# Performance work log

Hardware: AMD Instinct MI355X
Metric: run time of the kernel (lower is better)

## Reference

```python
import jax, jax.numpy as jnp
import numpy as np

N_NODES = 100000
EPS = 1e-6
NEG_SLOPE = 0.2


def setup_inputs() -> dict:
    key = jax.random.key(0)
    ks = jax.random.split(key, 7)
    N, E, IN, H, F = N_NODES, 1600000, 128, 4, 32
    feat = jax.random.normal(ks[0], (N, IN), dtype=jnp.float32)
    src = jax.random.randint(ks[1], (E,), 0, N, dtype=jnp.int32)
    dst = jax.random.randint(ks[2], (E,), 0, N, dtype=jnp.int32)
    # xavier-normal-ish scales (gain for relu = sqrt(2))
    W = jax.random.normal(ks[3], (IN, H * F), dtype=jnp.float32) * np.sqrt(2.0 * 2.0 / (IN + H * F)).astype(np.float32)
    attn_l = jax.random.normal(ks[4], (1, H, F), dtype=jnp.float32) * np.float32(np.sqrt(2.0 * 2.0 / (1 + F)))
    attn_r = jax.random.normal(ks[5], (1, H, F), dtype=jnp.float32) * np.float32(np.sqrt(2.0 * 2.0 / (1 + F)))
    bias = jnp.zeros((H * F,), dtype=jnp.float32)
    p = jax.random.normal(ks[6], (1,), dtype=jnp.float32)
    s_f = jnp.ones((1,), dtype=jnp.float32)
    return {"feat": feat, "src": src, "dst": dst, "W": W, "attn_l": attn_l,
            "attn_r": attn_r, "bias": bias, "p": p, "s_f": s_f}


def _leaky_relu(x, slope):
    return jnp.where(x >= 0, x, slope * x)


def reference(feat, src, dst, W, attn_l, attn_r, bias, p, s_f):
    N, H, F = feat.shape[0], attn_l.shape[1], attn_l.shape[2]
    # linear projection: [N, H, F]
    feat_proj = (feat @ W).reshape(N, H, F)
    # per-node attention logits: [N, H]
    el = jnp.sum(feat_proj * attn_l, axis=-1)
    er = jnp.sum(feat_proj * attn_r, axis=-1)
    # edge logits e = leaky_relu(el[src] + er[dst]) : [E, H]
    e = _leaky_relu(el[src] + er[dst], NEG_SLOPE)
    # edge softmax over incoming edges of each destination node
    emax = jax.ops.segment_max(e, dst, num_segments=N)        # [N, H]
    emax = jnp.where(jnp.isfinite(emax), emax, 0.0)
    e_exp = jnp.exp(e - emax[dst])                            # [E, H]
    denom = jax.ops.segment_sum(e_exp, dst, num_segments=N)   # [N, H]
    a = e_exp / (denom[dst] + 0.0)                            # [E, H]
    # power-mean aggregation
    p_eff = jax.nn.sigmoid(p[0]) + s_f[0]
    mu = feat_proj.min()
    pre_f = jnp.power(feat_proj - mu + EPS, p_eff)            # [N, H, F]
    msg = pre_f[src] * a[:, :, None]                          # [E, H, F]
    pre_rst = jax.ops.segment_sum(msg, dst, num_segments=N)   # [N, H, F]
    rst = jnp.power(pre_rst + EPS, 1.0 / p_eff) + mu
    rst = rst + bias.reshape(1, H, F)
    return rst.reshape(N, H * F)
```

## Files before the change

kernel.cpp:

```cpp
#include <hip/hip_runtime.h>
#include <hip/hip_fp16.h>
#include <math.h>

#define EPS 1e-6f
#define SLOPE 0.2f
#define NPART 8
#define BK 64

typedef __attribute__((ext_vector_type(8))) _Float16 f16x8;
typedef __attribute__((ext_vector_type(4))) float f32x4;

__device__ __forceinline__ unsigned fmap(float f) {
    unsigned b = __float_as_uint(f);
    return (b & 0x80000000u) ? ~b : (b | 0x80000000u);
}
__device__ __forceinline__ float funmap(unsigned m) {
    unsigned b = (m & 0x80000000u) ? (m ^ 0x80000000u) : ~m;
    return __uint_as_float(b);
}

__global__ __launch_bounds__(256) void gemm_mfma_kernel(
    const float* __restrict__ feat, const float* __restrict__ W,
    const float* __restrict__ attn_l, const float* __restrict__ attn_r,
    __half* __restrict__ fph, float* __restrict__ el, float* __restrict__ er,
    unsigned* __restrict__ mu_m, int N)
{
    __shared__ ushort Ald[128][136];
    __shared__ ushort Wld[128][136];
    __shared__ float red[256];

    int tid = threadIdx.x;
    int n0 = blockIdx.x * 128;

#pragma unroll
    for (int rep = 0; rep < 8; ++rep) {
        int slot = tid + rep * 256;
        int row = slot >> 4;
        int k8 = (slot & 15) << 3;
        int gr = n0 + row;
        uint4 u = make_uint4(0u, 0u, 0u, 0u);
        if (gr < N) {
            const float4* f4 = (const float4*)(feat + (size_t)gr * 128 + k8);
            float4 va = f4[0], vb = f4[1];
            __half2 p0 = __floats2half2_rn(va.x, va.y);
            __half2 p1 = __floats2half2_rn(va.z, va.w);
            __half2 p2 = __floats2half2_rn(vb.x, vb.y);
            __half2 p3 = __floats2half2_rn(vb.z, vb.w);
            u.x = *reinterpret_cast<unsigned*>(&p0);
            u.y = *reinterpret_cast<unsigned*>(&p1);
            u.z = *reinterpret_cast<unsigned*>(&p2);
            u.w = *reinterpret_cast<unsigned*>(&p3);
        }
        *(uint4*)&Ald[row][k8] = u;
    }
#pragma unroll
    for (int rep = 0; rep < 8; ++rep) {
        int slot = tid + rep * 256;
        int col = slot & 127;
        int k0 = (slot >> 7) << 3;
        ushort h[8];
#pragma unroll
        for (int j = 0; j < 8; ++j)
            h[j] = __half_as_ushort(__float2half_rn(W[(size_t)(k0 + j) * 128 + col]));
        *(uint4*)&Wld[col][k0] = *(uint4*)h;
    }
    __syncthreads();

    int lane = tid & 63;
    int wid = tid >> 6;
    int wr = wid >> 1, wc = wid & 1;
    int cl = lane & 15, g = lane >> 4;

    f32x4 acc[4][4];
#pragma unroll
    for (int i = 0; i < 4; i++)
#pragma unroll
        for (int j = 0; j < 4; j++) acc[i][j] = (f32x4){0.f, 0.f, 0.f, 0.f};

#pragma unroll
    for (int ks = 0; ks < 4; ++ks) {
        int kk = ks * 32 + g * 8;
        f16x8 aF[4], bF[4];
#pragma unroll
        for (int rt = 0; rt < 4; ++rt)
            aF[rt] = *(const f16x8*)&Ald[wr * 64 + rt * 16 + cl][kk];
#pragma unroll
        for (int ct = 0; ct < 4; ++ct)
            bF[ct] = *(const f16x8*)&Wld[wc * 64 + ct * 16 + cl][kk];
#pragma unroll
        for (int rt = 0; rt < 4; ++rt)
#pragma unroll
            for (int ct = 0; ct < 4; ++ct)
                acc[rt][ct] = __builtin_amdgcn_mfma_f32_16x16x32_f16(
                    aF[rt], bF[ct], acc[rt][ct], 0, 0, 0);
    }

    float alv[4], arv[4];
#pragma unroll
    for (int ct = 0; ct < 4; ++ct) {
        int h = (4 * wc + ct) >> 1;
        int f = ((ct & 1) << 4) + cl;
        alv[ct] = attn_l[h * 32 + f];
        arv[ct] = attn_r[h * 32 + f];
    }
#pragma unroll
    for (int rt = 0; rt < 4; ++rt) {
#pragma unroll
        for (int reg = 0; reg < 4; ++reg) {
            float e0 = acc[rt][0][reg] * alv[0] + acc[rt][1][reg] * alv[1];
            float e1 = acc[rt][2][reg] * alv[2] + acc[rt][3][reg] * alv[3];
            float r0 = acc[rt][0][reg] * arv[0] + acc[rt][1][reg] * arv[1];
            float r1 = acc[rt][2][reg] * arv[2] + acc[rt][3][reg] * arv[3];
#pragma unroll
            for (int m = 1; m < 16; m <<= 1) {
                e0 += __shfl_xor(e0, m);
                e1 += __shfl_xor(e1, m);
                r0 += __shfl_xor(r0, m);
                r1 += __shfl_xor(r1, m);
            }
            int R = n0 + wr * 64 + rt * 16 + g * 4 + reg;
            if (cl == 0 && R < N) {
                *(float2*)(el + (size_t)R * 4 + 2 * wc) = make_float2(e0, e1);
                *(float2*)(er + (size_t)R * 4 + 2 * wc) = make_float2(r0, r1);
            }
        }
    }

    float lmin = INFINITY;
#pragma unroll
    for (int rt = 0; rt < 4; ++rt)
#pragma unroll
        for (int reg = 0; reg < 4; ++reg) {
            int R = n0 + wr * 64 + rt * 16 + g * 4 + reg;
            if (R < N) {
#pragma unroll
                for (int ct = 0; ct < 4; ++ct) lmin = fminf(lmin, acc[rt][ct][reg]);
            }
        }
    red[tid] = lmin;
    __syncthreads();
    for (int s2 = 128; s2 > 0; s2 >>= 1) {
        if (tid < s2) red[tid] = fminf(red[tid], red[tid + s2]);
        __syncthreads();
    }
    if (tid == 0) atomicMin(mu_m, fmap(red[0]));

    __syncthreads();
    __half* hbuf = (__half*)&Ald[0][0];
#pragma unroll
    for (int rt = 0; rt < 4; ++rt)
#pragma unroll
        for (int ct = 0; ct < 4; ++ct)
#pragma unroll
            for (int reg = 0; reg < 4; ++reg) {
                int row = wr * 64 + rt * 16 + g * 4 + reg;
                int col = wc * 64 + ct * 16 + cl;
                hbuf[row * 136 + col] = __float2half_rn(acc[rt][ct][reg]);
            }
    __syncthreads();
    {
        int row = tid >> 1, seg = tid & 1;
        int gr = n0 + row;
        if (gr < N) {
            const uint4* s4 = (const uint4*)&Ald[row][seg * 64];
            uint4* d4 = (uint4*)(fph + (size_t)gr * 128 + seg * 64);
#pragma unroll
            for (int q = 0; q < 8; ++q) d4[q] = s4[q];
        }
    }
}

__global__ __launch_bounds__(256) void scatter_powp_kernel(
    const int* __restrict__ src, const int* __restrict__ dst,
    int* __restrict__ cnt, int* __restrict__ sorted_src,
    __half* __restrict__ fph, const unsigned* __restrict__ mu_m,
    const float* __restrict__ p, const float* __restrict__ s_f,
    int total8, int E, int N)
{
    {
        float mu = funmap(*mu_m);
        float pe = 1.f / (1.f + __expf(-p[0])) + s_f[0];
        int stride = gridDim.x * 256;
        for (int i = blockIdx.x * 256 + threadIdx.x; i < total8; i += stride) {
            uint4 u = *reinterpret_cast<uint4*>(fph + (size_t)i * 8);
            float2 f0 = __half22float2(*reinterpret_cast<__half2*>(&u.x));
            float2 f1 = __half22float2(*reinterpret_cast<__half2*>(&u.y));
            float2 f2 = __half22float2(*reinterpret_cast<__half2*>(&u.z));
            float2 f3 = __half22float2(*reinterpret_cast<__half2*>(&u.w));
            f0.x = __expf(pe * __logf(fmaxf(f0.x - mu, 0.f) + EPS));
            f0.y = __expf(pe * __logf(fmaxf(f0.y - mu, 0.f) + EPS));
            f1.x = __expf(pe * __logf(fmaxf(f1.x - mu, 0.f) + EPS));
            f1.y = __expf(pe * __logf(fmaxf(f1.y - mu, 0.f) + EPS));
            f2.x = __expf(pe * __logf(fmaxf(f2.x - mu, 0.f) + EPS));
            f2.y = __expf(pe * __logf(fmaxf(f2.y - mu, 0.f) + EPS));
            f3.x = __expf(pe * __logf(fmaxf(f3.x - mu, 0.f) + EPS));
            f3.y = __expf(pe * __logf(fmaxf(f3.y - mu, 0.f) + EPS));
            __half2 q0 = __floats2half2_rn(f0.x, f0.y);
            __half2 q1 = __floats2half2_rn(f1.x, f1.y);
            __half2 q2 = __floats2half2_rn(f2.x, f2.y);
            __half2 q3 = __floats2half2_rn(f3.x, f3.y);
            u.x = *reinterpret_cast<unsigned*>(&q0);
            u.y = *reinterpret_cast<unsigned*>(&q1);
            u.z = *reinterpret_cast<unsigned*>(&q2);
            u.w = *reinterpret_cast<unsigned*>(&q3);
            *reinterpret_cast<uint4*>(fph + (size_t)i * 8) = u;
        }
    }

    int grp = blockIdx.x & (NPART - 1);
    int R = (N + NPART - 1) / NPART;
    int lo = grp * R;
    int hi = min(N, lo + R);
    int E4 = E >> 2;
    int stride4 = (gridDim.x >> 3) * 256;
    const int4* dst4 = (const int4*)dst;
    const int4* src4 = (const int4*)src;
    for (int e4 = (blockIdx.x >> 3) * 256 + threadIdx.x; e4 < E4; e4 += stride4) {
        int4 d4 = dst4[e4];
        bool m0 = (d4.x >= lo) & (d4.x < hi);
        bool m1 = (d4.y >= lo) & (d4.y < hi);
        bool m2 = (d4.z >= lo) & (d4.z < hi);
        bool m3 = (d4.w >= lo) & (d4.w < hi);
        if (m0 | m1 | m2 | m3) {
            int4 s4 = src4[e4];
            if (m0) { int pos = atomicAdd(&cnt[d4.x], 1); if (pos < BK) sorted_src[(size_t)d4.x * BK + pos] = s4.x; }
            if (m1) { int pos = atomicAdd(&cnt[d4.y], 1); if (pos < BK) sorted_src[(size_t)d4.y * BK + pos] = s4.y; }
            if (m2) { int pos = atomicAdd(&cnt[d4.z], 1); if (pos < BK) sorted_src[(size_t)d4.z * BK + pos] = s4.z; }
            if (m3) { int pos = atomicAdd(&cnt[d4.w], 1); if (pos < BK) sorted_src[(size_t)d4.w * BK + pos] = s4.w; }
        }
    }
    if (blockIdx.x < NPART) {
        for (int e = E4 * 4 + threadIdx.x; e < E; e += 256) {
            int d = dst[e];
            if (d >= lo && d < hi) {
                int pos = atomicAdd(&cnt[d], 1);
                if (pos < BK) sorted_src[(size_t)d * BK + pos] = src[e];
            }
        }
    }
}

__global__ __launch_bounds__(256) void agg_kernel(
    const int* __restrict__ sorted_src, const int* __restrict__ cnt,
    const float* __restrict__ el, const float* __restrict__ er,
    const __half* __restrict__ fph, const float* __restrict__ bias,
    const unsigned* __restrict__ mu_m, const float* __restrict__ p,
    const float* __restrict__ s_f, float* __restrict__ out, int N)
{
    int node = blockIdx.x * 4 + (threadIdx.x >> 6);
    int lane = threadIdx.x & 63;
    if (node >= N) return;
    int esel = lane >> 3;
    int fb = lane & 7;
    int h = fb >> 1;
    float er_h = er[(size_t)node * 4 + h];

    int len = min(cnt[node], BK);
    int base = node * BK;

    float a[16];
#pragma unroll
    for (int q = 0; q < 16; q++) a[q] = 0.f;
    float dn = 0.f;

    for (int i = 0; i < len; i += 8) {
        int j = i + esel;
        bool valid = (j < len);
        int s = sorted_src[base + (valid ? j : i)];

        float x = el[(size_t)s * 4 + h] + er_h;
        x = x >= 0.f ? x : SLOPE * x;
        float w = valid ? __expf(x) : 0.f;
        uint4 u0 = *(const uint4*)(fph + (size_t)s * 128 + fb * 16);
        uint4 u1 = *(const uint4*)(fph + (size_t)s * 128 + fb * 16 + 8);
        dn += w;
        float2 gg;
        gg = __half22float2(*reinterpret_cast<__half2*>(&u0.x)); a[0]  = fmaf(w, gg.x, a[0]);  a[1]  = fmaf(w, gg.y, a[1]);
        gg = __half22float2(*reinterpret_cast<__half2*>(&u0.y)); a[2]  = fmaf(w, gg.x, a[2]);  a[3]  = fmaf(w, gg.y, a[3]);
        gg = __half22float2(*reinterpret_cast<__half2*>(&u0.z)); a[4]  = fmaf(w, gg.x, a[4]);  a[5]  = fmaf(w, gg.y, a[5]);
        gg = __half22float2(*reinterpret_cast<__half2*>(&u0.w)); a[6]  = fmaf(w, gg.x, a[6]);  a[7]  = fmaf(w, gg.y, a[7]);
        gg = __half22float2(*reinterpret_cast<__half2*>(&u1.x)); a[8]  = fmaf(w, gg.x, a[8]);  a[9]  = fmaf(w, gg.y, a[9]);
        gg = __half22float2(*reinterpret_cast<__half2*>(&u1.y)); a[10] = fmaf(w, gg.x, a[10]); a[11] = fmaf(w, gg.y, a[11]);
        gg = __half22float2(*reinterpret_cast<__half2*>(&u1.z)); a[12] = fmaf(w, gg.x, a[12]); a[13] = fmaf(w, gg.y, a[13]);
        gg = __half22float2(*reinterpret_cast<__half2*>(&u1.w)); a[14] = fmaf(w, gg.x, a[14]); a[15] = fmaf(w, gg.y, a[15]);
    }

#pragma unroll
    for (int q = 0; q < 16; q++) {
        a[q] += __shfl_xor(a[q], 8);
        a[q] += __shfl_xor(a[q], 16);
        a[q] += __shfl_xor(a[q], 32);
    }
    dn += __shfl_xor(dn, 8);
    dn += __shfl_xor(dn, 16);
    dn += __shfl_xor(dn, 32);

    if (esel == 0) {
        float mu = funmap(*mu_m);
        float pe = 1.f / (1.f + __expf(-p[0])) + s_f[0];
        float ip = 1.f / pe;
        float inv_dn = (len > 0) ? (1.f / dn) : 0.f;
        float o[16];
#pragma unroll
        for (int q = 0; q < 16; q++) {
            float b = bias[fb * 16 + q];
            o[q] = __expf(ip * __logf(fmaf(a[q], inv_dn, EPS))) + mu + b;
        }
        *(float4*)(out + (size_t)node * 128 + fb * 16)      = *(float4*)(&o[0]);
        *(float4*)(out + (size_t)node * 128 + fb * 16 + 4)  = *(float4*)(&o[4]);
        *(float4*)(out + (size_t)node * 128 + fb * 16 + 8)  = *(float4*)(&o[8]);
        *(float4*)(out + (size_t)node * 128 + fb * 16 + 12) = *(float4*)(&o[12]);
    }
}

extern "C" void kernel_launch(void* const* d_in, const int* in_sizes, int n_in,
                              void* d_out, int out_size, void* d_ws, size_t ws_size,
                              hipStream_t stream)
{
    const float* feat   = (const float*)d_in[0];
    const int*   src    = (const int*)d_in[1];
    const int*   dst    = (const int*)d_in[2];
    const float* W      = (const float*)d_in[3];
    const float* attn_l = (const float*)d_in[4];
    const float* attn_r = (const float*)d_in[5];
    const float* bias   = (const float*)d_in[6];
    const float* p      = (const float*)d_in[7];
    const float* s_f    = (const float*)d_in[8];
    float* out = (float*)d_out;

    const int N = in_sizes[0] / 128;
    const int E = in_sizes[1];

    char* ws = (char*)d_ws;
    size_t off = 0;
    auto alloc = [&](size_t bytes) -> char* {
        char* ptr = ws + off;
        off = (off + bytes + 255) & ~(size_t)255;
        return ptr;
    };
    __half*   fph        = (__half*)alloc((size_t)N * 128 * 2);
    float*    el         = (float*)alloc((size_t)N * 4 * 4);
    float*    er         = (float*)alloc((size_t)N * 4 * 4);
    int*      cnt        = (int*)alloc((size_t)N * 4);
    int*      sorted_src = (int*)alloc((size_t)N * BK * 4);
    unsigned* mu_m       = (unsigned*)alloc(256);

    hipMemsetAsync(cnt,  0,    (size_t)N * 4, stream);
    hipMemsetAsync(mu_m, 0xFF, 4,             stream);

    int total8 = N * 128 / 8;

    gemm_mfma_kernel<<<(N + 127) / 128, 256, 0, stream>>>(
        feat, W, attn_l, attn_r, fph, el, er, mu_m, N);
    scatter_powp_kernel<<<2048, 256, 0, stream>>>(src, dst, cnt, sorted_src,
                                                  fph, mu_m, p, s_f, total8, E, N);
    agg_kernel<<<(N + 3) / 4, 256, 0, stream>>>(sorted_src, cnt, el, er, fph,
                                                bias, mu_m, p, s_f, out, N);
}
```

Before: 219.6 us.

## Move edge bucketing into GEMM kernel and spread agg epilogue across all lanes

The dst-bucketed edge scatter moves out of the power kernel and into the tail of the GEMM kernel. It is independent of the projection, so it can overlap with the GEMM's compute-bound work, and the power kernel becomes a pure elementwise pass. In the aggregation kernel, the reduced accumulators go through shared memory so all 64 lanes, not just 8, each finish two output columns with log/exp and write coalesced float2 stores. Risks: the GEMM kernel's register and LDS pressure goes up, and it now runs ~782 blocks instead of 2048 for the scatter. Also, the shared fin buffer is read without a __syncthreads, relying on wave-level ordering within one wavefront.

```diff
diff --git a/kernel.cpp b/kernel.cpp
--- a/kernel.cpp
+++ b/kernel.cpp
@@ -19,11 +19,13 @@
     return __uint_as_float(b);
 }
 
-__global__ __launch_bounds__(256) void gemm_mfma_kernel(
+__global__ __launch_bounds__(256) void gemm_mfma_scatter_kernel(
     const float* __restrict__ feat, const float* __restrict__ W,
     const float* __restrict__ attn_l, const float* __restrict__ attn_r,
+    const int* __restrict__ src, const int* __restrict__ dst,
+    int* __restrict__ cnt, int* __restrict__ sorted_src,
     __half* __restrict__ fph, float* __restrict__ el, float* __restrict__ er,
-    unsigned* __restrict__ mu_m, int N)
+    unsigned* __restrict__ mu_m, int N, int E)
 {
     __shared__ ushort Ald[128][136];
     __shared__ ushort Wld[128][136];
@@ -168,75 +170,74 @@
             for (int q = 0; q < 8; ++q) d4[q] = s4[q];
         }
     }
-}
-
-__global__ __launch_bounds__(256) void scatter_powp_kernel(
-    const int* __restrict__ src, const int* __restrict__ dst,
-    int* __restrict__ cnt, int* __restrict__ sorted_src,
+
+    {
+        int grp = blockIdx.x & (NPART - 1);
+        int bg = blockIdx.x >> 3;
+        int count_g = (gridDim.x + 7 - grp) >> 3;
+        int R = (N + NPART - 1) / NPART;
+        int lo = grp * R;
+        int hi = min(N, lo + R);
+        int E4 = E >> 2;
+        int stride4 = count_g * 256;
+        const int4* dst4 = (const int4*)dst;
+        const int4* src4 = (const int4*)src;
+        for (int e4 = bg * 256 + tid; e4 < E4; e4 += stride4) {
+            int4 d4 = dst4[e4];
+            bool m0 = (d4.x >= lo) & (d4.x < hi);
+            bool m1 = (d4.y >= lo) & (d4.y < hi);
+            bool m2 = (d4.z >= lo) & (d4.z < hi);
+            bool m3 = (d4.w >= lo) & (d4.w < hi);
+            if (m0 | m1 | m2 | m3) {
+                int4 s4 = src4[e4];
+                if (m0) { int pos = atomicAdd(&cnt[d4.x], 1); if (pos < BK) sorted_src[(size_t)d4.x * BK + pos] = s4.x; }
+                if (m1) { int pos = atomicAdd(&cnt[d4.y], 1); if (pos < BK) sorted_src[(size_t)d4.y * BK + pos] = s4.y; }
+                if (m2) { int pos = atomicAdd(&cnt[d4.z], 1); if (pos < BK) sorted_src[(size_t)d4.z * BK + pos] = s4.z; }
+                if (m3) { int pos = atomicAdd(&cnt[d4.w], 1); if (pos < BK) sorted_src[(size_t)d4.w * BK + pos] = s4.w; }
+            }
+        }
+        if (bg == 0) {
+            for (int e = E4 * 4 + tid; e < E; e += 256) {
+                int d = dst[e];
+                if (d >= lo && d < hi) {
+                    int pos = atomicAdd(&cnt[d], 1);
+                    if (pos < BK) sorted_src[(size_t)d * BK + pos] = src[e];
+                }
+            }
+        }
+    }
+}
+
+__global__ __launch_bounds__(256) void powp_kernel(
     __half* __restrict__ fph, const unsigned* __restrict__ mu_m,
-    const float* __restrict__ p, const float* __restrict__ s_f,
-    int total8, int E, int N)
+    const float* __restrict__ p, const float* __restrict__ s_f, int total8)
 {
-    {
-        float mu = funmap(*mu_m);
-        float pe = 1.f / (1.f + __expf(-p[0])) + s_f[0];
-        int stride = gridDim.x * 256;
-        for (int i = blockIdx.x * 256 + threadIdx.x; i < total8; i += stride) {
-            uint4 u = *reinterpret_cast<uint4*>(fph + (size_t)i * 8);
-            float2 f0 = __half22float2(*reinterpret_cast<__half2*>(&u.x));
-            float2 f1 = __half22float2(*reinterpret_cast<__half2*>(&u.y));
-            float2 f2 = __half22float2(*reinterpret_cast<__half2*>(&u.z));
-            float2 f3 = __half22float2(*reinterpret_cast<__half2*>(&u.w));
-            f0.x = __expf(pe * __logf(fmaxf(f0.x - mu, 0.f) + EPS));
-            f0.y = __expf(pe * __logf(fmaxf(f0.y - mu, 0.f) + EPS));
-            f1.x = __expf(pe * __logf(fmaxf(f1.x - mu, 0.f) + EPS));
-            f1.y = __expf(pe * __logf(fmaxf(f1.y - mu, 0.f) + EPS));
-            f2.x = __expf(pe * __logf(fmaxf(f2.x - mu, 0.f) + EPS));
-            f2.y = __expf(pe * __logf(fmaxf(f2.y - mu, 0.f) + EPS));
-            f3.x = __expf(pe * __logf(fmaxf(f3.x - mu, 0.f) + EPS));
-            f3.y = __expf(pe * __logf(fmaxf(f3.y - mu, 0.f) + EPS));
-            __half2 q0 = __floats2half2_rn(f0.x, f0.y);
-            __half2 q1 = __floats2half2_rn(f1.x, f1.y);
-            __half2 q2 = __floats2half2_rn(f2.x, f2.y);
-            __half2 q3 = __floats2half2_rn(f3.x, f3.y);
-            u.x = *reinterpret_cast<unsigned*>(&q0);
-            u.y = *reinterpret_cast<unsigned*>(&q1);
-            u.z = *reinterpret_cast<unsigned*>(&q2);
-            u.w = *reinterpret_cast<unsigned*>(&q3);
-            *reinterpret_cast<uint4*>(fph + (size_t)i * 8) = u;
-        }
-    }
-
-    int grp = blockIdx.x & (NPART - 1);
-    int R = (N + NPART - 1) / NPART;
-    int lo = grp * R;
-    int hi = min(N, lo + R);
-    int E4 = E >> 2;
-    int stride4 = (gridDim.x >> 3) * 256;
-    const int4* dst4 = (const int4*)dst;
-    const int4* src4 = (const int4*)src;
-    for (int e4 = (blockIdx.x >> 3) * 256 + threadIdx.x; e4 < E4; e4 += stride4) {
-        int4 d4 = dst4[e4];
-        bool m0 = (d4.x >= lo) & (d4.x < hi);
-        bool m1 = (d4.y >= lo) & (d4.y < hi);
-        bool m2 = (d4.z >= lo) & (d4.z < hi);
-        bool m3 = (d4.w >= lo) & (d4.w < hi);
-        if (m0 | m1 | m2 | m3) {
-            int4 s4 = src4[e4];
-            if (m0) { int pos = atomicAdd(&cnt[d4.x], 1); if (pos < BK) sorted_src[(size_t)d4.x * BK + pos] = s4.x; }
-            if (m1) { int pos = atomicAdd(&cnt[d4.y], 1); if (pos < BK) sorted_src[(size_t)d4.y * BK + pos] = s4.y; }
-            if (m2) { int pos = atomicAdd(&cnt[d4.z], 1); if (pos < BK) sorted_src[(size_t)d4.z * BK + pos] = s4.z; }
-            if (m3) { int pos = atomicAdd(&cnt[d4.w], 1); if (pos < BK) sorted_src[(size_t)d4.w * BK + pos] = s4.w; }
-        }
-    }
-    if (blockIdx.x < NPART) {
-        for (int e = E4 * 4 + threadIdx.x; e < E; e += 256) {
-            int d = dst[e];
-            if (d >= lo && d < hi) {
-                int pos = atomicAdd(&cnt[d], 1);
-                if (pos < BK) sorted_src[(size_t)d * BK + pos] = src[e];
-            }
-        }
+    float mu = funmap(*mu_m);
+    float pe = 1.f / (1.f + __expf(-p[0])) + s_f[0];
+    int stride = gridDim.x * 256;
+    for (int i = blockIdx.x * 256 + threadIdx.x; i < total8; i += stride) {
+        uint4 u = *reinterpret_cast<uint4*>(fph + (size_t)i * 8);
+        float2 f0 = __half22float2(*reinterpret_cast<__half2*>(&u.x));
+        float2 f1 = __half22float2(*reinterpret_cast<__half2*>(&u.y));
+        float2 f2 = __half22float2(*reinterpret_cast<__half2*>(&u.z));
+        float2 f3 = __half22float2(*reinterpret_cast<__half2*>(&u.w));
+        f0.x = __expf(pe * __logf(fmaxf(f0.x - mu, 0.f) + EPS));
+        f0.y = __expf(pe * __logf(fmaxf(f0.y - mu, 0.f) + EPS));
+        f1.x = __expf(pe * __logf(fmaxf(f1.x - mu, 0.f) + EPS));
+        f1.y = __expf(pe * __logf(fmaxf(f1.y - mu, 0.f) + EPS));
+        f2.x = __expf(pe * __logf(fmaxf(f2.x - mu, 0.f) + EPS));
+        f2.y = __expf(pe * __logf(fmaxf(f2.y - mu, 0.f) + EPS));
+        f3.x = __expf(pe * __logf(fmaxf(f3.x - mu, 0.f) + EPS));
+        f3.y = __expf(pe * __logf(fmaxf(f3.y - mu, 0.f) + EPS));
+        __half2 q0 = __floats2half2_rn(f0.x, f0.y);
+        __half2 q1 = __floats2half2_rn(f1.x, f1.y);
+        __half2 q2 = __floats2half2_rn(f2.x, f2.y);
+        __half2 q3 = __floats2half2_rn(f3.x, f3.y);
+        u.x = *reinterpret_cast<unsigned*>(&q0);
+        u.y = *reinterpret_cast<unsigned*>(&q1);
+        u.z = *reinterpret_cast<unsigned*>(&q2);
+        u.w = *reinterpret_cast<unsigned*>(&q3);
+        *reinterpret_cast<uint4*>(fph + (size_t)i * 8) = u;
     }
 }
 
@@ -247,9 +248,11 @@
     const unsigned* __restrict__ mu_m, const float* __restrict__ p,
     const float* __restrict__ s_f, float* __restrict__ out, int N)
 {
+    __shared__ float fin[4][8][20];
     int node = blockIdx.x * 4 + (threadIdx.x >> 6);
     int lane = threadIdx.x & 63;
     if (node >= N) return;
+    int w = threadIdx.x >> 6;
     int esel = lane >> 3;
     int fb = lane & 7;
     int h = fb >> 1;
@@ -270,19 +273,19 @@
 
         float x = el[(size_t)s * 4 + h] + er_h;
         x = x >= 0.f ? x : SLOPE * x;
-        float w = valid ? __expf(x) : 0.f;
+        float wgt = valid ? __expf(x) : 0.f;
         uint4 u0 = *(const uint4*)(fph + (size_t)s * 128 + fb * 16);
         uint4 u1 = *(const uint4*)(fph + (size_t)s * 128 + fb * 16 + 8);
-        dn += w;
+        dn += wgt;
         float2 gg;
-        gg = __half22float2(*reinterpret_cast<__half2*>(&u0.x)); a[0]  = fmaf(w, gg.x, a[0]);  a[1]  = fmaf(w, gg.y, a[1]);
-        gg = __half22float2(*reinterpret_cast<__half2*>(&u0.y)); a[2]  = fmaf(w, gg.x, a[2]);  a[3]  = fmaf(w, gg.y, a[3]);
-        gg = __half22float2(*reinterpret_cast<__half2*>(&u0.z)); a[4]  = fmaf(w, gg.x, a[4]);  a[5]  = fmaf(w, gg.y, a[5]);
-        gg = __half22float2(*reinterpret_cast<__half2*>(&u0.w)); a[6]  = fmaf(w, gg.x, a[6]);  a[7]  = fmaf(w, gg.y, a[7]);
-        gg = __half22float2(*reinterpret_cast<__half2*>(&u1.x)); a[8]  = fmaf(w, gg.x, a[8]);  a[9]  = fmaf(w, gg.y, a[9]);
-        gg = __half22float2(*reinterpret_cast<__half2*>(&u1.y)); a[10] = fmaf(w, gg.x, a[10]); a[11] = fmaf(w, gg.y, a[11]);
-        gg = __half22float2(*reinterpret_cast<__half2*>(&u1.z)); a[12] = fmaf(w, gg.x, a[12]); a[13] = fmaf(w, gg.y, a[13]);
-        gg = __half22float2(*reinterpret_cast<__half2*>(&u1.w)); a[14] = fmaf(w, gg.x, a[14]); a[15] = fmaf(w, gg.y, a[15]);
+        gg = __half22float2(*reinterpret_cast<__half2*>(&u0.x)); a[0]  = fmaf(wgt, gg.x, a[0]);  a[1]  = fmaf(wgt, gg.y, a[1]);
+        gg = __half22float2(*reinterpret_cast<__half2*>(&u0.y)); a[2]  = fmaf(wgt, gg.x, a[2]);  a[3]  = fmaf(wgt, gg.y, a[3]);
+        gg = __half22float2(*reinterpret_cast<__half2*>(&u0.z)); a[4]  = fmaf(wgt, gg.x, a[4]);  a[5]  = fmaf(wgt, gg.y, a[5]);
+        gg = __half22float2(*reinterpret_cast<__half2*>(&u0.w)); a[6]  = fmaf(wgt, gg.x, a[6]);  a[7]  = fmaf(wgt, gg.y, a[7]);
+        gg = __half22float2(*reinterpret_cast<__half2*>(&u1.x)); a[8]  = fmaf(wgt, gg.x, a[8]);  a[9]  = fmaf(wgt, gg.y, a[9]);
+        gg = __half22float2(*reinterpret_cast<__half2*>(&u1.y)); a[10] = fmaf(wgt, gg.x, a[10]); a[11] = fmaf(wgt, gg.y, a[11]);
+        gg = __half22float2(*reinterpret_cast<__half2*>(&u1.z)); a[12] = fmaf(wgt, gg.x, a[12]); a[13] = fmaf(wgt, gg.y, a[13]);
+        gg = __half22float2(*reinterpret_cast<__half2*>(&u1.w)); a[14] = fmaf(wgt, gg.x, a[14]); a[15] = fmaf(wgt, gg.y, a[15]);
     }
 
 #pragma unroll
@@ -296,21 +299,27 @@
     dn += __shfl_xor(dn, 32);
 
     if (esel == 0) {
-        float mu = funmap(*mu_m);
-        float pe = 1.f / (1.f + __expf(-p[0])) + s_f[0];
-        float ip = 1.f / pe;
-        float inv_dn = (len > 0) ? (1.f / dn) : 0.f;
-        float o[16];
-#pragma unroll
-        for (int q = 0; q < 16; q++) {
-            float b = bias[fb * 16 + q];
-            o[q] = __expf(ip * __logf(fmaf(a[q], inv_dn, EPS))) + mu + b;
-        }
-        *(float4*)(out + (size_t)node * 128 + fb * 16)      = *(float4*)(&o[0]);
-        *(float4*)(out + (size_t)node * 128 + fb * 16 + 4)  = *(float4*)(&o[4]);
-        *(float4*)(out + (size_t)node * 128 + fb * 16 + 8)  = *(float4*)(&o[8]);
-        *(float4*)(out + (size_t)node * 128 + fb * 16 + 12) = *(float4*)(&o[12]);
-    }
+        *(float4*)&fin[w][fb][0]  = *(float4*)&a[0];
+        *(float4*)&fin[w][fb][4]  = *(float4*)&a[4];
+        *(float4*)&fin[w][fb][8]  = *(float4*)&a[8];
+        *(float4*)&fin[w][fb][12] = *(float4*)&a[12];
+        fin[w][fb][16] = dn;
+    }
+    int c = lane * 2;
+    int sfb = lane >> 3;
+    int q0 = c & 15;
+    float2 av = *(float2*)&fin[w][sfb][q0];
+    float dnv = fin[w][sfb][16];
+
+    float mu = funmap(*mu_m);
+    float pe = 1.f / (1.f + __expf(-p[0])) + s_f[0];
+    float ip = 1.f / pe;
+    float inv_dn = (len > 0) ? (1.f / dnv) : 0.f;
+    float2 b2 = *(const float2*)(bias + c);
+    float2 o;
+    o.x = __expf(ip * __logf(fmaf(av.x, inv_dn, EPS))) + mu + b2.x;
+    o.y = __expf(ip * __logf(fmaf(av.y, inv_dn, EPS))) + mu + b2.y;
+    *(float2*)(out + (size_t)node * 128 + c) = o;
 }
 
 extern "C" void kernel_launch(void* const* d_in, const int* in_sizes, int n_in,
@@ -350,10 +359,9 @@
 
     int total8 = N * 128 / 8;
 
-    gemm_mfma_kernel<<<(N + 127) / 128, 256, 0, stream>>>(
-        feat, W, attn_l, attn_r, fph, el, er, mu_m, N);
-    scatter_powp_kernel<<<2048, 256, 0, stream>>>(src, dst, cnt, sorted_src,
-                                                  fph, mu_m, p, s_f, total8, E, N);
+    gemm_mfma_scatter_kernel<<<(N + 127) / 128, 256, 0, stream>>>(
+        feat, W, attn_l, attn_r, src, dst, cnt, sorted_src, fph, el, er, mu_m, N, E);
+    powp_kernel<<<2048, 256, 0, stream>>>(fph, mu_m, p, s_f, total8);
     agg_kernel<<<(N + 3) / 4, 256, 0, stream>>>(sorted_src, cnt, el, er, fph,
                                                 bias, mu_m, p, s_f, out, N);
 }
```

Measured after the change: 225.3 us. +2.6%, slower.
